# Optimization experiments

Measured on AMD Instinct MI355X. Metric: run time of the kernel, lower is better.

Reference implementation:

```python
import jax, jax.numpy as jnp
import numpy as np

N, DEG, F_IN, F_OUT = 100000, 16, 128, 128
E = N * DEG


def setup_inputs() -> dict:
    key = jax.random.key(0)
    k0, k1, k2, k3 = jax.random.split(key, 4)
    x = jax.random.normal(k0, (N, F_IN), dtype=jnp.float32)
    # ragged neighbor list flattened: each node has DEG neighbors (sorted segment ids)
    neighbor_feats = jax.random.normal(k1, (E, F_IN), dtype=jnp.float32)
    segment_ids = jnp.repeat(jnp.arange(N, dtype=jnp.int32), DEG)
    # nn.Linear(in, out, bias=False) weights, stored [out, in] as in torch
    Wx = jax.random.normal(k2, (F_OUT, F_IN), dtype=jnp.float32) / np.float32(np.sqrt(F_IN))
    Wn = jax.random.normal(k3, (F_OUT, F_IN), dtype=jnp.float32) / np.float32(np.sqrt(F_IN))
    return {"x": x, "neighbor_feats": neighbor_feats, "segment_ids": segment_ids,
            "Wx": Wx, "Wn": Wn}


def reference(x, neighbor_feats, segment_ids, Wx, Wn):
    n_nodes = x.shape[0]
    # MeanAggregator: per-node mean over its neighbor rows (segment mean)
    sums = jax.ops.segment_sum(neighbor_feats, segment_ids, num_segments=n_nodes)
    counts = jax.ops.segment_sum(
        jnp.ones((neighbor_feats.shape[0],), dtype=x.dtype), segment_ids,
        num_segments=n_nodes)
    f = sums / jnp.maximum(counts, 1.0)[:, None]  # [N, F_IN]
    # tranx(x) + trann(f)
    x_out = x @ Wx.T + f @ Wn.T                   # [N, F_OUT]
    # neighbor = [tranx(n) for n in neighbor], flattened
    nb_out = neighbor_feats @ Wx.T                # [E, F_OUT]
    return x_out, nb_out
```

## Files before the change

kernel.cpp:

```cpp
#include <hip/hip_runtime.h>
#include <stdint.h>
#include <stddef.h>

#define N_NODES 100000
#define F_DIM   128
#define DEG     16
#define N_EDGES (N_NODES*DEG)
#define ROWS_PER_TILE 128
#define N_TILES (N_EDGES/ROWS_PER_TILE)
#define NODES_PER_TILE (ROWS_PER_TILE/DEG)
#define GRID_BLOCKS 2500
#define TILES_PER_BLOCK (N_TILES/GRID_BLOCKS)
#define BLOCK_THREADS 256
#define G_STRIDE 132

typedef __bf16 bf16;
typedef __bf16 bf16x8 __attribute__((ext_vector_type(8)));
typedef float  f32x4  __attribute__((ext_vector_type(4)));

__device__ __forceinline__ int swz(int row, int col) {
  return row*128 + (col ^ ((row & 7) << 3));
}

__device__ __forceinline__ bf16x8 cvt8(f32x4 a, f32x4 b) {
  bf16x8 v;
  v[0]=(bf16)a[0]; v[1]=(bf16)a[1]; v[2]=(bf16)a[2]; v[3]=(bf16)a[3];
  v[4]=(bf16)b[0]; v[5]=(bf16)b[1]; v[6]=(bf16)b[2]; v[7]=(bf16)b[3];
  return v;
}

__device__ __forceinline__ bf16x8 load_frag_g(const float* __restrict__ p) {
  f32x4 a = *(const f32x4*)p;
  f32x4 b = *(const f32x4*)(p + 4);
  return cvt8(a, b);
}

__global__ __launch_bounds__(BLOCK_THREADS, 2)
void feattrans_kernel(const float* __restrict__ x,
                      const float* __restrict__ nb,
                      const float* __restrict__ Wx,
                      const float* __restrict__ Wn,
                      float* __restrict__ out)
{
  __shared__ bf16  w_lds[2*128*128];
  __shared__ float g_lds[2][NODES_PER_TILE][G_STRIDE];

  const int tid  = threadIdx.x;
  const int wave = tid >> 6;
  const int lane = tid & 63;
  const int l15  = lane & 15;
  const int lk   = lane >> 4;

  #pragma unroll
  for (int it = 0; it < 16; ++it) {
    int idx = it * BLOCK_THREADS + tid;
    int mat = idx >> 11;
    int rem = idx & 2047;
    int row = rem >> 4;
    int g   = rem & 15;
    const float* src = (mat ? Wn : Wx) + row*128 + g*8;
    bf16x8 v = load_frag_g(src);
    *(bf16x8*)&w_lds[mat*16384 + swz(row, g*8)] = v;
  }
  __syncthreads();

  float* out_x  = out;
  float* out_nb = out + (size_t)N_NODES * F_DIM;

  const int bid = blockIdx.x;

  bf16x8 afr[2][2][4];

  {
    const size_t erow0 = (size_t)bid * ROWS_PER_TILE;
    #pragma unroll
    for (int mt = 0; mt < 2; ++mt)
      #pragma unroll
      for (int ks = 0; ks < 4; ++ks)
        afr[0][mt][ks] = load_frag_g(nb + (erow0 + wave*32 + mt*16 + l15) * F_DIM + ks*32 + lk*8);
  }

  #pragma unroll
  for (int t = 0; t < TILES_PER_BLOCK; ++t) {
    const int cur = t & 1, nxt = cur ^ 1;
    const int tile = bid + t * GRID_BLOCKS;
    const size_t erow0 = (size_t)tile * ROWS_PER_TILE;
    const int nodebase = tile * NODES_PER_TILE;

    int xrow = nodebase + l15;
    if (xrow > N_NODES - 1) xrow = N_NODES - 1;
    bf16x8 xfr[4];
    #pragma unroll
    for (int ks = 0; ks < 4; ++ks)
      xfr[ks] = load_frag_g(x + (size_t)xrow * F_DIM + ks*32 + lk*8);

    f32x4 acc[2][8] = {};
    #pragma unroll
    for (int nt = 0; nt < 8; ++nt) {
      #pragma unroll
      for (int ks = 0; ks < 4; ++ks) {
        bf16x8 bfr = *(bf16x8*)&w_lds[swz(nt*16 + l15, ks*32 + lk*8)];
        acc[0][nt] = __builtin_amdgcn_mfma_f32_16x16x32_bf16(bfr, afr[cur][0][ks], acc[0][nt], 0, 0, 0);
        acc[1][nt] = __builtin_amdgcn_mfma_f32_16x16x32_bf16(bfr, afr[cur][1][ks], acc[1][nt], 0, 0, 0);
      }
    }
    #pragma unroll
    for (int mt = 0; mt < 2; ++mt)
      #pragma unroll
      for (int nt = 0; nt < 8; ++nt)
        *(f32x4*)(out_nb + (erow0 + wave*32 + mt*16 + l15) * F_DIM + nt*16 + lk*4) = acc[mt][nt];

    #pragma unroll
    for (int mt = 0; mt < 2; ++mt) {
      f32x4 a2[8] = {};
      #pragma unroll
      for (int nt = 0; nt < 8; ++nt)
        #pragma unroll
        for (int ks = 0; ks < 4; ++ks) {
          bf16x8 bfr = *(bf16x8*)&w_lds[16384 + swz(nt*16 + l15, ks*32 + lk*8)];
          a2[nt] = __builtin_amdgcn_mfma_f32_16x16x32_bf16(afr[cur][mt][ks], bfr, a2[nt], 0, 0, 0);
        }
      const int gnode = 2*wave + mt;
      #pragma unroll
      for (int nt = 0; nt < 8; ++nt) {
        float s = a2[nt][0] + a2[nt][1] + a2[nt][2] + a2[nt][3];
        s += __shfl_xor(s, 16, 64);
        s += __shfl_xor(s, 32, 64);
        s *= (1.0f / DEG);
        if (lk == (nt >> 1))
          g_lds[cur][gnode][nt*16 + l15] = s;
      }
    }

    if (t < TILES_PER_BLOCK - 1) {
      const size_t erowN = erow0 + (size_t)GRID_BLOCKS * ROWS_PER_TILE;
      #pragma unroll
      for (int mt = 0; mt < 2; ++mt)
        #pragma unroll
        for (int ks = 0; ks < 4; ++ks)
          afr[nxt][mt][ks] = load_frag_g(nb + (erowN + wave*32 + mt*16 + l15) * F_DIM + ks*32 + lk*8);
    }

    __syncthreads();

    f32x4 xacc[2] = {};
    #pragma unroll
    for (int j = 0; j < 2; ++j) {
      const int nt = 2*wave + j;
      #pragma unroll
      for (int ks = 0; ks < 4; ++ks) {
        bf16x8 bx = *(bf16x8*)&w_lds[swz(nt*16 + l15, ks*32 + lk*8)];
        xacc[j] = __builtin_amdgcn_mfma_f32_16x16x32_bf16(bx, xfr[ks], xacc[j], 0, 0, 0);
      }
    }
    if (l15 < NODES_PER_TILE) {
      #pragma unroll
      for (int j = 0; j < 2; ++j) {
        const int nt = 2*wave + j;
        f32x4 g4 = *(f32x4*)&g_lds[cur][l15][nt*16 + lk*4];
        f32x4 v  = xacc[j] + g4;
        *(f32x4*)(out_x + (size_t)(nodebase + l15) * F_DIM + nt*16 + lk*4) = v;
      }
    }
  }
}

extern "C" void kernel_launch(void* const* d_in, const int* in_sizes, int n_in,
                              void* d_out, int out_size, void* d_ws, size_t ws_size,
                              hipStream_t stream) {
  const float* x  = (const float*)d_in[0];
  const float* nb = (const float*)d_in[1];
  const float* Wx = (const float*)d_in[3];
  const float* Wn = (const float*)d_in[4];
  float* out = (float*)d_out;

  feattrans_kernel<<<dim3(GRID_BLOCKS), dim3(BLOCK_THREADS), 0, stream>>>(x, nb, Wx, Wn, out);
}
```

Baseline: 356.4 us.

## Switch to persistent 512-block grid with ping-pong tile loop and merged MFMA chains

```diff
diff --git a/kernel.cpp b/kernel.cpp
--- a/kernel.cpp
+++ b/kernel.cpp
@@ -9,8 +9,7 @@
 #define ROWS_PER_TILE 128
 #define N_TILES (N_EDGES/ROWS_PER_TILE)
 #define NODES_PER_TILE (ROWS_PER_TILE/DEG)
-#define GRID_BLOCKS 2500
-#define TILES_PER_BLOCK (N_TILES/GRID_BLOCKS)
+#define GRID_BLOCKS 512
 #define BLOCK_THREADS 256
 #define G_STRIDE 132
 
@@ -33,6 +32,89 @@
   f32x4 a = *(const f32x4*)p;
   f32x4 b = *(const f32x4*)(p + 4);
   return cvt8(a, b);
+}
+
+#define TILE_BODY(TILE, AC, AN, GB, PF)                                        \
+{                                                                              \
+  const size_t erow0_ = (size_t)(TILE) * ROWS_PER_TILE;                        \
+  const int nodebase_ = (TILE) * NODES_PER_TILE;                               \
+              \
+  const int xrow_ = nodebase_ + (l15 & 7);                                     \
+  bf16x8 xfr_[4];                                                              \
+  _Pragma("unroll")                                                            \
+  for (int ks = 0; ks < 4; ++ks)                                               \
+    xfr_[ks] = load_frag_g(x + (size_t)xrow_ * F_DIM + ks*32 + lk*8);          \
+                    \
+  f32x4 acc_[2][8] = {};                                                       \
+  _Pragma("unroll")                                                            \
+  for (int nt = 0; nt < 8; ++nt) {                                             \
+    _Pragma("unroll")                                                          \
+    for (int ks = 0; ks < 4; ++ks) {                                           \
+      bf16x8 bfr = *(bf16x8*)&w_lds[swz(nt*16 + l15, ks*32 + lk*8)];           \
+      acc_[0][nt] = __builtin_amdgcn_mfma_f32_16x16x32_bf16(bfr, AC[0][ks], acc_[0][nt], 0, 0, 0); \
+      acc_[1][nt] = __builtin_amdgcn_mfma_f32_16x16x32_bf16(bfr, AC[1][ks], acc_[1][nt], 0, 0, 0); \
+    }                                                                          \
+  }                                                                            \
+  _Pragma("unroll")                                                            \
+  for (int mt = 0; mt < 2; ++mt)                                               \
+    _Pragma("unroll")                                                          \
+    for (int nt = 0; nt < 8; ++nt)                                             \
+      *(f32x4*)(out_nb + (erow0_ + wave*32 + mt*16 + l15) * F_DIM + nt*16 + lk*4) = acc_[mt][nt]; \
+               \
+  f32x4 a2_[2][8] = {};                                                        \
+  _Pragma("unroll")                                                            \
+  for (int nt = 0; nt < 8; ++nt) {                                             \
+    _Pragma("unroll")                                                          \
+    for (int ks = 0; ks < 4; ++ks) {                                           \
+      bf16x8 bfr = *(bf16x8*)&w_lds[16384 + swz(nt*16 + l15, ks*32 + lk*8)];   \
+      a2_[0][nt] = __builtin_amdgcn_mfma_f32_16x16x32_bf16(AC[0][ks], bfr, a2_[0][nt], 0, 0, 0); \
+      a2_[1][nt] = __builtin_amdgcn_mfma_f32_16x16x32_bf16(AC[1][ks], bfr, a2_[1][nt], 0, 0, 0); \
+    }                                                                          \
+  }                                                                            \
+                                             \
+  _Pragma("unroll")                                                            \
+  for (int mt = 0; mt < 2; ++mt) {                                             \
+    const int gnode_ = 2*wave + mt;                                            \
+    _Pragma("unroll")                                                          \
+    for (int nt = 0; nt < 8; ++nt) {                                           \
+      float s = a2_[mt][nt][0] + a2_[mt][nt][1] + a2_[mt][nt][2] + a2_[mt][nt][3]; \
+      s += __shfl_xor(s, 16, 64);                                              \
+      s += __shfl_xor(s, 32, 64);                                              \
+      s *= (1.0f / DEG);                                                       \
+      if (lk == (nt >> 1)) GB[gnode_][nt*16 + l15] = s;                        \
+    }                                                                          \
+  }                                                                            \
+                \
+  if (PF) {                                                                    \
+    const size_t erowN_ = erow0_ + (size_t)GRID_BLOCKS * ROWS_PER_TILE;        \
+    _Pragma("unroll")                                                          \
+    for (int mt = 0; mt < 2; ++mt)                                             \
+      _Pragma("unroll")                                                        \
+      for (int ks = 0; ks < 4; ++ks)                                           \
+        AN[mt][ks] = load_frag_g(nb + (erowN_ + wave*32 + mt*16 + l15) * F_DIM + ks*32 + lk*8); \
+  }                                                                            \
+  __syncthreads();                  \
+        \
+  f32x4 xacc_[2] = {};                                                         \
+  _Pragma("unroll")                                                            \
+  for (int j = 0; j < 2; ++j) {                                                \
+    const int nt = 2*wave + j;                                                 \
+    _Pragma("unroll")                                                          \
+    for (int ks = 0; ks < 4; ++ks) {                                           \
+      bf16x8 bx = *(bf16x8*)&w_lds[swz(nt*16 + l15, ks*32 + lk*8)];            \
+      xacc_[j] = __builtin_amdgcn_mfma_f32_16x16x32_bf16(bx, xfr_[ks], xacc_[j], 0, 0, 0); \
+    }                                                                          \
+  }                                                                            \
+  if (l15 < NODES_PER_TILE) {                                                  \
+    _Pragma("unroll")                                                          \
+    for (int j = 0; j < 2; ++j) {                                              \
+      const int nt = 2*wave + j;                                               \
+      f32x4 g4 = *(f32x4*)&GB[l15][nt*16 + lk*4];                              \
+      f32x4 v  = xacc_[j] + g4;                                                \
+      *(f32x4*)(out_x + (size_t)(nodebase_ + l15) * F_DIM + nt*16 + lk*4) = v; \
+    }                                                                          \
+  }                                                                            \
+          \
 }
 
 __global__ __launch_bounds__(BLOCK_THREADS, 2)
@@ -69,7 +151,7 @@
 
   const int bid = blockIdx.x;
 
-  bf16x8 afr[2][2][4];
+  bf16x8 afr0[2][4], afr1[2][4];
 
   {
     const size_t erow0 = (size_t)bid * ROWS_PER_TILE;
@@ -77,91 +159,22 @@
     for (int mt = 0; mt < 2; ++mt)
       #pragma unroll
       for (int ks = 0; ks < 4; ++ks)
-        afr[0][mt][ks] = load_frag_g(nb + (erow0 + wave*32 + mt*16 + l15) * F_DIM + ks*32 + lk*8);
+        afr0[mt][ks] = load_frag_g(nb + (erow0 + wave*32 + mt*16 + l15) * F_DIM + ks*32 + lk*8);
   }
 
-  #pragma unroll
-  for (int t = 0; t < TILES_PER_BLOCK; ++t) {
-    const int cur = t & 1, nxt = cur ^ 1;
-    const int tile = bid + t * GRID_BLOCKS;
-    const size_t erow0 = (size_t)tile * ROWS_PER_TILE;
-    const int nodebase = tile * NODES_PER_TILE;
+  int tile = bid;
+  while (true) {
+    const int tileB = tile + GRID_BLOCKS;
+    const bool hasB = (tileB < N_TILES);
+    TILE_BODY(tile, afr0, afr1, g_lds[0], hasB);
+    if (!hasB) break;
 
-    int xrow = nodebase + l15;
-    if (xrow > N_NODES - 1) xrow = N_NODES - 1;
-    bf16x8 xfr[4];
-    #pragma unroll
-    for (int ks = 0; ks < 4; ++ks)
-      xfr[ks] = load_frag_g(x + (size_t)xrow * F_DIM + ks*32 + lk*8);
+    const int tileC = tileB + GRID_BLOCKS;
+    const bool hasC = (tileC < N_TILES);
+    TILE_BODY(tileB, afr1, afr0, g_lds[1], hasC);
+    if (!hasC) break;
 
-    f32x4 acc[2][8] = {};
-    #pragma unroll
-    for (int nt = 0; nt < 8; ++nt) {
-      #pragma unroll
-      for (int ks = 0; ks < 4; ++ks) {
-        bf16x8 bfr = *(bf16x8*)&w_lds[swz(nt*16 + l15, ks*32 + lk*8)];
-        acc[0][nt] = __builtin_amdgcn_mfma_f32_16x16x32_bf16(bfr, afr[cur][0][ks], acc[0][nt], 0, 0, 0);
-        acc[1][nt] = __builtin_amdgcn_mfma_f32_16x16x32_bf16(bfr, afr[cur][1][ks], acc[1][nt], 0, 0, 0);
-      }
-    }
-    #pragma unroll
-    for (int mt = 0; mt < 2; ++mt)
-      #pragma unroll
-      for (int nt = 0; nt < 8; ++nt)
-        *(f32x4*)(out_nb + (erow0 + wave*32 + mt*16 + l15) * F_DIM + nt*16 + lk*4) = acc[mt][nt];
-
-    #pragma unroll
-    for (int mt = 0; mt < 2; ++mt) {
-      f32x4 a2[8] = {};
-      #pragma unroll
-      for (int nt = 0; nt < 8; ++nt)
-        #pragma unroll
-        for (int ks = 0; ks < 4; ++ks) {
-          bf16x8 bfr = *(bf16x8*)&w_lds[16384 + swz(nt*16 + l15, ks*32 + lk*8)];
-          a2[nt] = __builtin_amdgcn_mfma_f32_16x16x32_bf16(afr[cur][mt][ks], bfr, a2[nt], 0, 0, 0);
-        }
-      const int gnode = 2*wave + mt;
-      #pragma unroll
-      for (int nt = 0; nt < 8; ++nt) {
-        float s = a2[nt][0] + a2[nt][1] + a2[nt][2] + a2[nt][3];
-        s += __shfl_xor(s, 16, 64);
-        s += __shfl_xor(s, 32, 64);
-        s *= (1.0f / DEG);
-        if (lk == (nt >> 1))
-          g_lds[cur][gnode][nt*16 + l15] = s;
-      }
-    }
-
-    if (t < TILES_PER_BLOCK - 1) {
-      const size_t erowN = erow0 + (size_t)GRID_BLOCKS * ROWS_PER_TILE;
-      #pragma unroll
-      for (int mt = 0; mt < 2; ++mt)
-        #pragma unroll
-        for (int ks = 0; ks < 4; ++ks)
-          afr[nxt][mt][ks] = load_frag_g(nb + (erowN + wave*32 + mt*16 + l15) * F_DIM + ks*32 + lk*8);
-    }
-
-    __syncthreads();
-
-    f32x4 xacc[2] = {};
-    #pragma unroll
-    for (int j = 0; j < 2; ++j) {
-      const int nt = 2*wave + j;
-      #pragma unroll
-      for (int ks = 0; ks < 4; ++ks) {
-        bf16x8 bx = *(bf16x8*)&w_lds[swz(nt*16 + l15, ks*32 + lk*8)];
-        xacc[j] = __builtin_amdgcn_mfma_f32_16x16x32_bf16(bx, xfr[ks], xacc[j], 0, 0, 0);
-      }
-    }
-    if (l15 < NODES_PER_TILE) {
-      #pragma unroll
-      for (int j = 0; j < 2; ++j) {
-        const int nt = 2*wave + j;
-        f32x4 g4 = *(f32x4*)&g_lds[cur][l15][nt*16 + lk*4];
-        f32x4 v  = xacc[j] + g4;
-        *(f32x4*)(out_x + (size_t)(nodebase + l15) * F_DIM + nt*16 + lk*4) = v;
-      }
-    }
+    tile = tileC;
   }
 }
 
```

Result: no change. 362.3 us (+1.7%).
